# Optimization experiments

Hardware: AMD Instinct MI355X
Metric: run time of the kernel (lower is better)

The kernel has to match this reference:

```python
import jax, jax.numpy as jnp
import numpy as np
from jax import lax

BN_EPS = 1e-5


def ste_sign(t):
    # sign() binarization with straight-through estimator (identity grad),
    # matching BinarizeConv2d which binarizes .data in-place.
    return t + lax.stop_gradient(jnp.sign(t) - t)


def setup_inputs() -> dict:
    key = jax.random.key(0)
    k1, k2, k3, k4 = jax.random.split(key, 4)
    N, C, H, W = 128, 256, 28, 28
    x = jax.random.normal(k1, (N, C, H, W), dtype=jnp.float32)
    w = jax.random.normal(k2, (C, C, 3, 3), dtype=jnp.float32)  # OIHW
    gamma = jnp.ones((C,), dtype=jnp.float32)
    beta = jnp.zeros((C,), dtype=jnp.float32)
    running_mean = jax.random.normal(k3, (C,), dtype=jnp.float32)
    running_var = jax.random.uniform(k4, (C,), dtype=jnp.float32)
    return {"x": x, "w": w, "gamma": gamma, "beta": beta,
            "running_mean": running_mean, "running_var": running_var}


def reference(x, w, gamma, beta, running_mean, running_var):
    residual = x
    # Binarize activations and weights to {-1, 0, +1} via sign (0 measure-zero for randn)
    xb = ste_sign(x)
    wb = ste_sign(w)
    # 3x3 conv, stride 1, padding 1, no bias
    out = lax.conv_general_dilated(
        xb, wb, window_strides=(1, 1), padding=((1, 1), (1, 1)),
        dimension_numbers=("NCHW", "OIHW", "NCHW"))
    # BatchNorm2d (inference form with running stats), per-channel affine
    inv = gamma / jnp.sqrt(running_var + BN_EPS)  # [C]
    out = out * inv[None, :, None, None] + (beta - running_mean * inv)[None, :, None, None]
    # Hardtanh
    out = jnp.clip(out, -1.0, 1.0)
    # residual add (downsample is None)
    return out + residual
```

## Files before the change

### kernel.cpp

```cpp
#include <hip/hip_runtime.h>
#include <stdint.h>

typedef unsigned long long u64;

#define N_ 128
#define C_ 256
#define H_ 28
#define W_ 28
#define BN_EPS_ 1e-5f

__global__ __launch_bounds__(256) void pack_x_kernel(const float* __restrict__ x,
                                                     u64* __restrict__ xbits) {
    int nh = blockIdx.x;
    int h  = nh % H_;
    int n  = nh / H_;
    __shared__ float sx[C_][W_ + 1];

    const float* xplane = x + ((size_t)n * C_ * H_ + h) * W_;
    for (int i = threadIdx.x; i < C_ * 7; i += 256) {
        int c = i / 7, q = i - c * 7;
        float4 v = *(const float4*)(xplane + (size_t)c * (H_ * W_) + q * 4);
        sx[c][q * 4 + 0] = v.x;
        sx[c][q * 4 + 1] = v.y;
        sx[c][q * 4 + 2] = v.z;
        sx[c][q * 4 + 3] = v.w;
    }
    __syncthreads();

    int k    = threadIdx.x >> 6;
    int lane = threadIdx.x & 63;
    int c    = k * 64 + lane;
    u64 my = 0;
    #pragma unroll
    for (int w = 0; w < W_; ++w) {
        u64 mask = __ballot(sx[c][w] < 0.f);
        if (lane == w) my = mask;
    }
    if (lane < W_) xbits[((size_t)nh * W_ + lane) * 4 + k] = my;
}

__global__ __launch_bounds__(256) void pack_w_kernel(const float* __restrict__ w,
                                                     u64* __restrict__ wbits) {
    int gid  = blockIdx.x * blockDim.x + threadIdx.x;
    int wave = gid >> 6;
    int lane = gid & 63;
    if (wave >= C_ * 9 * 4) return;
    int k    = wave & 3;
    int rest = wave >> 2;
    int tap  = rest % 9;
    int co   = rest / 9;
    int ci   = k * 64 + lane;
    float val = w[((size_t)co * C_ + ci) * 9 + tap];
    u64 mask = __ballot(val < 0.f);
    if (lane == 0) wbits[wave] = mask;
}

__global__ __launch_bounds__(256, 2) void conv_kernel(
    const u64* __restrict__ xbits, const u64* __restrict__ wbits,
    const float* __restrict__ x,
    const float* __restrict__ gamma, const float* __restrict__ beta,
    const float* __restrict__ mean, const float* __restrict__ var,
    float* __restrict__ out) {
    int nh = blockIdx.x;
    int h  = nh % H_;
    int n  = nh / H_;
    int co = threadIdx.x;

    __shared__ u64   lx[3][W_][4];
    __shared__ float sout[C_][W_ + 1];

    float inv  = gamma[co] / sqrtf(var[co] + BN_EPS_);
    float bias = beta[co] - mean[co] * inv;

    u64 wr[9][4];
    {
        const ulonglong2* wp = (const ulonglong2*)wbits + (size_t)co * 18;
        #pragma unroll
        for (int i = 0; i < 9; ++i) {
            ulonglong2 a = wp[i * 2];
            ulonglong2 b = wp[i * 2 + 1];
            wr[i][0] = a.x; wr[i][1] = a.y; wr[i][2] = b.x; wr[i][3] = b.y;
        }
    }

    for (int i = threadIdx.x; i < 3 * W_ * 4; i += 256) {
        int k    = i & 3;
        int rest = i >> 2;
        int ww   = rest % W_;
        int r    = rest / W_;
        int ih   = h - 1 + r;
        u64 v = 0;
        if (ih >= 0 && ih < H_)
            v = xbits[(((size_t)n * H_ + ih) * W_ + ww) * 4 + k];
        lx[r][ww][k] = v;
    }
    __syncthreads();

    const bool row0 = (h > 0);
    const bool row2 = (h < H_ - 1);
    const int  nrows = 1 + (row0 ? 1 : 0) + (row2 ? 1 : 0);
    const int  nv3 = C_ * nrows * 3;
    const int  nv2 = C_ * nrows * 2;

    int pm = 0, pc = 0;

    for (int iw = 0; iw < W_; ++iw) {
        int a0 = 0, a1 = 0, a2 = 0;
        u64 xw0, xw1, xw2, xw3;
        #define TAPROW(r, wb)                                                  \
            xw0 = lx[r][iw][0]; xw1 = lx[r][iw][1];                            \
            xw2 = lx[r][iw][2]; xw3 = lx[r][iw][3];                            \
            a0 += __popcll(xw0 ^ wr[wb+0][0]) + __popcll(xw1 ^ wr[wb+0][1]) +  \
                  __popcll(xw2 ^ wr[wb+0][2]) + __popcll(xw3 ^ wr[wb+0][3]);   \
            a1 += __popcll(xw0 ^ wr[wb+1][0]) + __popcll(xw1 ^ wr[wb+1][1]) +  \
                  __popcll(xw2 ^ wr[wb+1][2]) + __popcll(xw3 ^ wr[wb+1][3]);   \
            a2 += __popcll(xw0 ^ wr[wb+2][0]) + __popcll(xw1 ^ wr[wb+2][1]) +  \
                  __popcll(xw2 ^ wr[wb+2][2]) + __popcll(xw3 ^ wr[wb+2][3]);
        if (row0) { TAPROW(0, 0) }
        { TAPROW(1, 3) }
        if (row2) { TAPROW(2, 6) }
        #undef TAPROW

        if (iw >= 1) {
            int s  = pm + a2;
            int nv = (iw == 1) ? nv2 : nv3;
            float val = (float)(nv - 2 * s) * inv + bias;
            val = fminf(1.f, fmaxf(-1.f, val));
            sout[co][iw - 1] = val;
        }
        pm = pc + a1;
        pc = a0;
    }
    {
        float val = (float)(nv2 - 2 * pm) * inv + bias;
        val = fminf(1.f, fmaxf(-1.f, val));
        sout[co][W_ - 1] = val;
    }
    __syncthreads();

    const float* xplane = x   + ((size_t)n * C_ * H_ + h) * W_;
    float*       oplane = out + ((size_t)n * C_ * H_ + h) * W_;
    for (int i = threadIdx.x; i < C_ * W_; i += 256) {
        int c    = i / W_;
        int wpos = i - c * W_;
        size_t g = (size_t)c * (H_ * W_) + wpos;
        oplane[g] = sout[c][wpos] + xplane[g];
    }
}

extern "C" void kernel_launch(void* const* d_in, const int* in_sizes, int n_in,
                              void* d_out, int out_size, void* d_ws, size_t ws_size,
                              hipStream_t stream) {
    const float* x     = (const float*)d_in[0];
    const float* w     = (const float*)d_in[1];
    const float* gamma = (const float*)d_in[2];
    const float* beta  = (const float*)d_in[3];
    const float* mean  = (const float*)d_in[4];
    const float* var   = (const float*)d_in[5];
    float* out = (float*)d_out;

    u64* xbits = (u64*)d_ws;
    u64* wbits = xbits + (size_t)N_ * H_ * W_ * 4;

    pack_x_kernel<<<N_ * H_, 256, 0, stream>>>(x, xbits);
    pack_w_kernel<<<(C_ * 9 * 4 * 64) / 256, 256, 0, stream>>>(w, wbits);
    conv_kernel<<<N_ * H_, 256, 0, stream>>>(xbits, wbits, x, gamma, beta, mean, var, out);
}
```

Baseline: 328.8 us.

## Split conv channel reduction across thread pairs and vectorize epilogue stores

The conv kernel now launches 512 threads per block, with two threads per output channel. Each thread handles half of the 256 input-channel bits and the pair combines partial sums with a shuffle-xor. Halving the weight registers per thread is meant to raise occupancy and give more parallelism to hide popcount and LDS latency. The residual epilogue now uses float4 loads and stores. The costs are the extra shuffles, redundant BN math in both threads of a pair, and a row loop unrolled by 4.

```diff
diff --git a/kernel.cpp b/kernel.cpp
--- a/kernel.cpp
+++ b/kernel.cpp
@@ -8,6 +8,7 @@
 #define H_ 28
 #define W_ 28
 #define BN_EPS_ 1e-5f
+
 
 __global__ __launch_bounds__(256) void pack_x_kernel(const float* __restrict__ x,
                                                      u64* __restrict__ xbits) {
@@ -55,7 +56,7 @@
     if (lane == 0) wbits[wave] = mask;
 }
 
-__global__ __launch_bounds__(256, 2) void conv_kernel(
+__global__ __launch_bounds__(512, 4) void conv_kernel(
     const u64* __restrict__ xbits, const u64* __restrict__ wbits,
     const float* __restrict__ x,
     const float* __restrict__ gamma, const float* __restrict__ beta,
@@ -64,7 +65,8 @@
     int nh = blockIdx.x;
     int h  = nh % H_;
     int n  = nh / H_;
-    int co = threadIdx.x;
+    int co = threadIdx.x >> 1;
+    int kh = threadIdx.x & 1;
 
     __shared__ u64   lx[3][W_][4];
     __shared__ float sout[C_][W_ + 1];
@@ -72,18 +74,18 @@
     float inv  = gamma[co] / sqrtf(var[co] + BN_EPS_);
     float bias = beta[co] - mean[co] * inv;
 
-    u64 wr[9][4];
+    u64 wr[9][2];
     {
-        const ulonglong2* wp = (const ulonglong2*)wbits + (size_t)co * 18;
+        const u64* wp = wbits + (size_t)co * 36 + kh * 2;
         #pragma unroll
-        for (int i = 0; i < 9; ++i) {
-            ulonglong2 a = wp[i * 2];
-            ulonglong2 b = wp[i * 2 + 1];
-            wr[i][0] = a.x; wr[i][1] = a.y; wr[i][2] = b.x; wr[i][3] = b.y;
+        for (int t = 0; t < 9; ++t) {
+            ulonglong2 a = *(const ulonglong2*)(wp + t * 4);
+            wr[t][0] = a.x; wr[t][1] = a.y;
         }
     }
 
-    for (int i = threadIdx.x; i < 3 * W_ * 4; i += 256) {
+    if (threadIdx.x < 3 * W_ * 4) {
+        int i    = threadIdx.x;
         int k    = i & 3;
         int rest = i >> 2;
         int ww   = rest % W_;
@@ -104,47 +106,52 @@
 
     int pm = 0, pc = 0;
 
+    #pragma unroll 4
     for (int iw = 0; iw < W_; ++iw) {
         int a0 = 0, a1 = 0, a2 = 0;
-        u64 xw0, xw1, xw2, xw3;
+        ulonglong2 xr;
         #define TAPROW(r, wb)                                                  \
-            xw0 = lx[r][iw][0]; xw1 = lx[r][iw][1];                            \
-            xw2 = lx[r][iw][2]; xw3 = lx[r][iw][3];                            \
-            a0 += __popcll(xw0 ^ wr[wb+0][0]) + __popcll(xw1 ^ wr[wb+0][1]) +  \
-                  __popcll(xw2 ^ wr[wb+0][2]) + __popcll(xw3 ^ wr[wb+0][3]);   \
-            a1 += __popcll(xw0 ^ wr[wb+1][0]) + __popcll(xw1 ^ wr[wb+1][1]) +  \
-                  __popcll(xw2 ^ wr[wb+1][2]) + __popcll(xw3 ^ wr[wb+1][3]);   \
-            a2 += __popcll(xw0 ^ wr[wb+2][0]) + __popcll(xw1 ^ wr[wb+2][1]) +  \
-                  __popcll(xw2 ^ wr[wb+2][2]) + __popcll(xw3 ^ wr[wb+2][3]);
+            xr = *(const ulonglong2*)&lx[r][iw][kh * 2];                       \
+            a0 += __popcll(xr.x ^ wr[wb+0][0]) + __popcll(xr.y ^ wr[wb+0][1]); \
+            a1 += __popcll(xr.x ^ wr[wb+1][0]) + __popcll(xr.y ^ wr[wb+1][1]); \
+            a2 += __popcll(xr.x ^ wr[wb+2][0]) + __popcll(xr.y ^ wr[wb+2][1]);
         if (row0) { TAPROW(0, 0) }
         { TAPROW(1, 3) }
         if (row2) { TAPROW(2, 6) }
         #undef TAPROW
 
         if (iw >= 1) {
-            int s  = pm + a2;
+            int s = pm + a2;
+            s += __shfl_xor(s, 1);
             int nv = (iw == 1) ? nv2 : nv3;
             float val = (float)(nv - 2 * s) * inv + bias;
             val = fminf(1.f, fmaxf(-1.f, val));
-            sout[co][iw - 1] = val;
+            if (kh == 0) sout[co][iw - 1] = val;
         }
         pm = pc + a1;
         pc = a0;
     }
     {
-        float val = (float)(nv2 - 2 * pm) * inv + bias;
+        int s = pm;
+        s += __shfl_xor(s, 1);
+        float val = (float)(nv2 - 2 * s) * inv + bias;
         val = fminf(1.f, fmaxf(-1.f, val));
-        sout[co][W_ - 1] = val;
+        if (kh == 0) sout[co][W_ - 1] = val;
     }
     __syncthreads();
 
     const float* xplane = x   + ((size_t)n * C_ * H_ + h) * W_;
     float*       oplane = out + ((size_t)n * C_ * H_ + h) * W_;
-    for (int i = threadIdx.x; i < C_ * W_; i += 256) {
-        int c    = i / W_;
-        int wpos = i - c * W_;
-        size_t g = (size_t)c * (H_ * W_) + wpos;
-        oplane[g] = sout[c][wpos] + xplane[g];
+    for (int i = threadIdx.x; i < C_ * 7; i += 512) {
+        int c = i / 7, q = i - c * 7;
+        size_t g = (size_t)c * (H_ * W_) + q * 4;
+        float4 r = *(const float4*)(xplane + g);
+        float4 o;
+        o.x = sout[c][q * 4 + 0] + r.x;
+        o.y = sout[c][q * 4 + 1] + r.y;
+        o.z = sout[c][q * 4 + 2] + r.z;
+        o.w = sout[c][q * 4 + 3] + r.w;
+        *(float4*)(oplane + g) = o;
     }
 }
 
@@ -164,5 +171,5 @@
 
     pack_x_kernel<<<N_ * H_, 256, 0, stream>>>(x, xbits);
     pack_w_kernel<<<(C_ * 9 * 4 * 64) / 256, 256, 0, stream>>>(w, wbits);
-    conv_kernel<<<N_ * H_, 256, 0, stream>>>(xbits, wbits, x, gamma, beta, mean, var, out);
+    conv_kernel<<<N_ * H_, 512, 0, stream>>>(xbits, wbits, x, gamma, beta, mean, var, out);
 }
```

New measurement: 320.7 us. 2.5% less time.

## Remap binary conv so lanes own pixels and loop over output channels

Applied to the files above, without the earlier changes.

The conv kernel now assigns each lane a spatial pixel, with two rows of 28 packed into 56 active lanes. It loops over 64 output channels per wave, loading their weight bits as wave-uniform values, and uses lane shuffles to combine the horizontal taps. Padding is handled with popcount corrections at the edges, and the shared-memory staging and transposed output buffer are removed. Lanes 56-63 of each wave sit idle, and the output stores are strided by channel but coalesced per row.

```diff
diff --git a/kernel.cpp b/kernel.cpp
--- a/kernel.cpp
+++ b/kernel.cpp
@@ -7,6 +7,7 @@
 #define C_ 256
 #define H_ 28
 #define W_ 28
+#define HP_ (H_ / 2)
 #define BN_EPS_ 1e-5f
 
 __global__ __launch_bounds__(256) void pack_x_kernel(const float* __restrict__ x,
@@ -55,96 +56,110 @@
     if (lane == 0) wbits[wave] = mask;
 }
 
-__global__ __launch_bounds__(256, 2) void conv_kernel(
+__global__ __launch_bounds__(128, 4) void conv_kernel(
     const u64* __restrict__ xbits, const u64* __restrict__ wbits,
     const float* __restrict__ x,
     const float* __restrict__ gamma, const float* __restrict__ beta,
     const float* __restrict__ mean, const float* __restrict__ var,
     float* __restrict__ out) {
-    int nh = blockIdx.x;
-    int h  = nh % H_;
-    int n  = nh / H_;
-    int co = threadIdx.x;
 
-    __shared__ u64   lx[3][W_][4];
-    __shared__ float sout[C_][W_ + 1];
+    int bx = blockIdx.x;
+    int hp = bx % HP_;
+    int n  = bx / HP_;
+    int wv = __builtin_amdgcn_readfirstlane(threadIdx.x >> 6);
+    int ls = threadIdx.x & 63;
+    int co_base = (blockIdx.y * 2 + wv) * 64;
 
-    float inv  = gamma[co] / sqrtf(var[co] + BN_EPS_);
-    float bias = beta[co] - mean[co] * inv;
+    bool active = ls < 56;
+    int h_sub = (active && ls >= 28) ? 1 : 0;
+    int w     = active ? (ls - h_sub * 28) : 0;
+    int h     = hp * 2 + h_sub;
 
-    u64 wr[9][4];
+    float invV, biasV;
     {
-        const ulonglong2* wp = (const ulonglong2*)wbits + (size_t)co * 18;
-        #pragma unroll
-        for (int i = 0; i < 9; ++i) {
-            ulonglong2 a = wp[i * 2];
-            ulonglong2 b = wp[i * 2 + 1];
-            wr[i][0] = a.x; wr[i][1] = a.y; wr[i][2] = b.x; wr[i][3] = b.y;
-        }
+        int cj = co_base + ls;
+        float iv = gamma[cj] / sqrtf(var[cj] + BN_EPS_);
+        invV  = iv;
+        biasV = beta[cj] - mean[cj] * iv;
     }
 
-    for (int i = threadIdx.x; i < 3 * W_ * 4; i += 256) {
-        int k    = i & 3;
-        int rest = i >> 2;
-        int ww   = rest % W_;
-        int r    = rest / W_;
-        int ih   = h - 1 + r;
-        u64 v = 0;
-        if (ih >= 0 && ih < H_)
-            v = xbits[(((size_t)n * H_ + ih) * W_ + ww) * 4 + k];
-        lx[r][ww][k] = v;
+    const bool wL = (w > 0), wR = (w < W_ - 1);
+    int nrows  = 1 + (h > 0 ? 1 : 0) + (h < H_ - 1 ? 1 : 0);
+    int ncols  = 1 + (wL ? 1 : 0) + (wR ? 1 : 0);
+    int nvalid = C_ * nrows * ncols;
+
+    u64 xr[3][4];
+    #pragma unroll
+    for (int r = 0; r < 3; ++r) {
+        int ih = h - 1 + r;
+        bool v = (ih >= 0) && (ih < H_);
+        const ulonglong2* p = (const ulonglong2*)(
+            xbits + (((size_t)n * H_ + (v ? ih : 0)) * W_ + w) * 4);
+        ulonglong2 a, b;
+        if (v) { a = p[0]; b = p[1]; }
+        else   { a.x = a.y = b.x = b.y = 0ull; }
+        xr[r][0] = a.x; xr[r][1] = a.y; xr[r][2] = b.x; xr[r][3] = b.y;
     }
-    __syncthreads();
 
-    const bool row0 = (h > 0);
-    const bool row2 = (h < H_ - 1);
-    const int  nrows = 1 + (row0 ? 1 : 0) + (row2 ? 1 : 0);
-    const int  nv3 = C_ * nrows * 3;
-    const int  nv2 = C_ * nrows * 2;
+    const bool edgeTop = (hp == 0);
+    const bool edgeBot = (hp == HP_ - 1);
 
-    int pm = 0, pc = 0;
+    size_t base = ((size_t)n * C_ + co_base) * (H_ * W_) + (size_t)h * W_ + w;
+    const float* xp = x + base;
+    float*       op = out + base;
 
-    for (int iw = 0; iw < W_; ++iw) {
-        int a0 = 0, a1 = 0, a2 = 0;
-        u64 xw0, xw1, xw2, xw3;
-        #define TAPROW(r, wb)                                                  \
-            xw0 = lx[r][iw][0]; xw1 = lx[r][iw][1];                            \
-            xw2 = lx[r][iw][2]; xw3 = lx[r][iw][3];                            \
-            a0 += __popcll(xw0 ^ wr[wb+0][0]) + __popcll(xw1 ^ wr[wb+0][1]) +  \
-                  __popcll(xw2 ^ wr[wb+0][2]) + __popcll(xw3 ^ wr[wb+0][3]);   \
-            a1 += __popcll(xw0 ^ wr[wb+1][0]) + __popcll(xw1 ^ wr[wb+1][1]) +  \
-                  __popcll(xw2 ^ wr[wb+1][2]) + __popcll(xw3 ^ wr[wb+1][3]);   \
-            a2 += __popcll(xw0 ^ wr[wb+2][0]) + __popcll(xw1 ^ wr[wb+2][1]) +  \
-                  __popcll(xw2 ^ wr[wb+2][2]) + __popcll(xw3 ^ wr[wb+2][3]);
-        if (row0) { TAPROW(0, 0) }
-        { TAPROW(1, 3) }
-        if (row2) { TAPROW(2, 6) }
-        #undef TAPROW
+    for (int j = 0; j < 64; ++j) {
+        const u64* wsp = wbits + (size_t)(co_base + j) * 36;
+        u64 ws[9][4];
+        #pragma unroll
+        for (int t = 0; t < 9; ++t) {
+            #pragma unroll
+            for (int k = 0; k < 4; ++k) ws[t][k] = wsp[t * 4 + k];
+        }
 
-        if (iw >= 1) {
-            int s  = pm + a2;
-            int nv = (iw == 1) ? nv2 : nv3;
-            float val = (float)(nv - 2 * s) * inv + bias;
-            val = fminf(1.f, fmaxf(-1.f, val));
-            sout[co][iw - 1] = val;
+        float res = *xp;
+
+        int A0 = 0, A1 = 0, A2 = 0;
+        #pragma unroll
+        for (int r = 0; r < 3; ++r) {
+            #pragma unroll
+            for (int k = 0; k < 4; ++k) {
+                u64 xv = xr[r][k];
+                A0 += (int)__popcll(xv ^ ws[r * 3 + 0][k]);
+                A1 += (int)__popcll(xv ^ ws[r * 3 + 1][k]);
+                A2 += (int)__popcll(xv ^ ws[r * 3 + 2][k]);
+            }
         }
-        pm = pc + a1;
-        pc = a0;
-    }
-    {
-        float val = (float)(nv2 - 2 * pm) * inv + bias;
+        int upA0 = __shfl_up(A0, 1);
+        int dnA2 = __shfl_down(A2, 1);
+        int S = A1 + (wL ? upA0 : 0) + (wR ? dnA2 : 0);
+
+        int B = nvalid;
+        if (edgeTop | edgeBot) {
+            int corr = 0;
+            if (edgeTop && h == 0) {
+                int P0 = (int)(__popcll(ws[0][0]) + __popcll(ws[0][1]) + __popcll(ws[0][2]) + __popcll(ws[0][3]));
+                int P1 = (int)(__popcll(ws[1][0]) + __popcll(ws[1][1]) + __popcll(ws[1][2]) + __popcll(ws[1][3]));
+                int P2 = (int)(__popcll(ws[2][0]) + __popcll(ws[2][1]) + __popcll(ws[2][2]) + __popcll(ws[2][3]));
+                corr = P1 + (wL ? P0 : 0) + (wR ? P2 : 0);
+            }
+            if (edgeBot && h == H_ - 1) {
+                int P6 = (int)(__popcll(ws[6][0]) + __popcll(ws[6][1]) + __popcll(ws[6][2]) + __popcll(ws[6][3]));
+                int P7 = (int)(__popcll(ws[7][0]) + __popcll(ws[7][1]) + __popcll(ws[7][2]) + __popcll(ws[7][3]));
+                int P8 = (int)(__popcll(ws[8][0]) + __popcll(ws[8][1]) + __popcll(ws[8][2]) + __popcll(ws[8][3]));
+                corr = P7 + (wL ? P6 : 0) + (wR ? P8 : 0);
+            }
+            B += 2 * corr;
+        }
+
+        float inv  = __shfl(invV, j);
+        float bias = __shfl(biasV, j);
+        float val = (float)(B - 2 * S) * inv + bias;
         val = fminf(1.f, fmaxf(-1.f, val));
-        sout[co][W_ - 1] = val;
-    }
-    __syncthreads();
+        if (active) *op = val + res;
 
-    const float* xplane = x   + ((size_t)n * C_ * H_ + h) * W_;
-    float*       oplane = out + ((size_t)n * C_ * H_ + h) * W_;
-    for (int i = threadIdx.x; i < C_ * W_; i += 256) {
-        int c    = i / W_;
-        int wpos = i - c * W_;
-        size_t g = (size_t)c * (H_ * W_) + wpos;
-        oplane[g] = sout[c][wpos] + xplane[g];
+        xp += H_ * W_;
+        op += H_ * W_;
     }
 }
 
@@ -164,5 +179,6 @@
 
     pack_x_kernel<<<N_ * H_, 256, 0, stream>>>(x, xbits);
     pack_w_kernel<<<(C_ * 9 * 4 * 64) / 256, 256, 0, stream>>>(w, wbits);
-    conv_kernel<<<N_ * H_, 256, 0, stream>>>(xbits, wbits, x, gamma, beta, mean, var, out);
+    conv_kernel<<<dim3(N_ * HP_, 2), 128, 0, stream>>>(xbits, wbits, x, gamma, beta,
+                                                       mean, var, out);
 }
```

Result: slower. 346.1 us (+5.3%).
